# Kernel optimization log

Hardware: AMD Instinct MI355X
Metric: run time of the kernel (lower is better)

Reference implementation:

```python
import jax, jax.numpy as jnp
import numpy as np

B, N, D, K = 32, 2048, 512, 256
NEG_SLOPE = 0.01  # torch LeakyReLU default


def setup_inputs() -> dict:
    key = jax.random.key(0)
    k1, k2, k3, k4, k5, k6 = jax.random.split(key, 6)
    s = 1.0 / np.sqrt(D)
    sk = 1.0 / np.sqrt(K)
    return {
        "vI": jax.random.normal(k1, (B, N, D), dtype=jnp.float32),
        "vQ": jax.random.normal(k2, (B, D), dtype=jnp.float32),
        "Wi": jax.random.uniform(k3, (D, K), minval=-s, maxval=s, dtype=jnp.float32),
        "Wq": jax.random.uniform(k4, (D, K), minval=-s, maxval=s, dtype=jnp.float32),
        "bq": jax.random.uniform(k5, (K,), minval=-s, maxval=s, dtype=jnp.float32),
        "Wp": jax.random.uniform(k6, (K, 1), minval=-sk, maxval=sk, dtype=jnp.float32),
        "bp": jnp.zeros((1,), dtype=jnp.float32),
    }


def reference(vI, vQ, Wi, Wq, bq, Wp, bp):
    # vI: [B,N,D], vQ: [B,D]
    vIp = jnp.einsum("bnd,dk->bnk", vI, Wi)          # [B,N,K] (no bias)
    vQp = vQ @ Wq + bq                                  # [B,K]
    ha = jax.nn.leaky_relu(vIp + vQp[:, None, :], NEG_SLOPE)  # [B,N,K]
    scores = jnp.einsum("bnk,k->bn", ha, Wp[:, 0]) + bp[0]    # [B,N]
    pi = jax.nn.softmax(scores, axis=-1)                # [B,N]
    vI_attn = jnp.einsum("bn,bnk->bk", pi, vIp)        # [B,K]
    return vI_attn + vQp
```

## Files before the change

### kernel.cpp

```cpp
#include <hip/hip_runtime.h>

#define CB 32
#define CN 2048
#define CD 512
#define CK 256

typedef __bf16 bf16x8 __attribute__((ext_vector_type(8)));
typedef float  f32x4  __attribute__((ext_vector_type(4)));

__device__ __forceinline__ unsigned pk2bf(float a, float b) {
    union { float f; unsigned u; } x, y; x.f = a; y.f = b;
    unsigned ru = x.u + 0x7fffu + ((x.u >> 16) & 1u);
    unsigned rv = y.u + 0x7fffu + ((y.u >> 16) & 1u);
    return (ru >> 16) | (rv & 0xffff0000u);
}

__device__ __forceinline__ unsigned short bf16r(float a) {
    union { float f; unsigned u; } x; x.f = a;
    unsigned r = x.u + 0x7fffu + ((x.u >> 16) & 1u);
    return (unsigned short)(r >> 16);
}

__device__ __forceinline__ void glds16(const void* g, void* l) {
    __builtin_amdgcn_global_load_lds(
        (const __attribute__((address_space(1))) void*)g,
        (__attribute__((address_space(3))) void*)l, 16, 0, 0);
}

__global__ __launch_bounds__(256) void prep_kernel(
        const float* __restrict__ Wi, const float* __restrict__ Wq,
        const float* __restrict__ vQ, const float* __restrict__ bq,
        unsigned short* __restrict__ WiT, float* __restrict__ vQpP)
{
    const int tid = threadIdx.x;
    if (blockIdx.x < 32) {
        const int t = blockIdx.x;
        const int d0 = (t >> 2) * 64, k0 = (t & 3) * 64;
        __shared__ float sT[64][68];
        const int r = tid >> 4, c4 = (tid & 15) * 4;
        #pragma unroll
        for (int i = 0; i < 4; ++i) {
            float4 v = *reinterpret_cast<const float4*>(
                Wi + (size_t)(d0 + r + i * 16) * CK + k0 + c4);
            *reinterpret_cast<float4*>(&sT[r + i * 16][c4]) = v;
        }
        __syncthreads();
        const int k = tid >> 2, dg = (tid & 3) * 16;
        unsigned short __attribute__((aligned(16))) ov[16];
        #pragma unroll
        for (int j = 0; j < 16; ++j) ov[j] = bf16r(sT[dg + j][k]);
        unsigned short* dst = WiT + (size_t)(k0 + k) * CD + d0 + dg;
        *reinterpret_cast<uint4*>(dst)     = *reinterpret_cast<const uint4*>(&ov[0]);
        *reinterpret_cast<uint4*>(dst + 8) = *reinterpret_cast<const uint4*>(&ov[8]);
    } else {
        const int bb = blockIdx.x - 32;
        const int b = bb >> 3, j = bb & 7;
        __shared__ float sq[64];
        if (tid < 64) sq[tid] = vQ[b * CD + j * 64 + tid];
        __syncthreads();
        float acc = (j == 0) ? bq[tid] : 0.f;
        const float* wq = Wq + (size_t)j * 64 * CK + tid;
        #pragma unroll
        for (int d = 0; d < 64; d += 8) {
            float wv[8];
            #pragma unroll
            for (int u = 0; u < 8; ++u) wv[u] = wq[(d + u) * CK];
            #pragma unroll
            for (int u = 0; u < 8; ++u) acc += sq[d + u] * wv[u];
        }
        vQpP[(size_t)bb * CK + tid] = acc;
    }
}

__global__ __launch_bounds__(256, 2) void scores_fused_kernel(
        const float* __restrict__ vI, const unsigned short* __restrict__ WiT,
        const float* __restrict__ vQpP, const float* __restrict__ Wp,
        float* __restrict__ numP, float* __restrict__ Zp, float* __restrict__ mP)
{
    constexpr int BM = 128, BK = 64;
    __shared__ __align__(16) unsigned short sB[2][CK * BK];
    float* fb   = (float*)sB[0];
    float* svq  = fb;
    float* swp  = fb + 256;
    float* sS   = fb + 512;
    float* sW   = fb + 640;
    float* snum = fb + 768;

    const int tid  = threadIdx.x;
    const int b    = blockIdx.y;
    const int n0   = blockIdx.x * BM;
    const int wave = tid >> 6;
    const int lane = tid & 63;
    const int col  = lane & 15;
    const int quad = lane >> 4;

    const float* vIb   = vI + ((size_t)b * CN + n0) * CD;
    const float* aBase = vIb + (size_t)(wave * 32 + col) * CD + quad * 8;

    int gBoff[8];
    #pragma unroll
    for (int i = 0; i < 8; ++i) {
        int row = wave * 64 + i * 8 + (lane >> 3);
        int c   = (lane & 7) ^ (row & 7);
        gBoff[i] = row * CD + c * 8;
    }

    f32x4 acc[2][16];
    #pragma unroll
    for (int mt = 0; mt < 2; ++mt)
        #pragma unroll
        for (int kt = 0; kt < 16; ++kt)
            acc[mt][kt] = (f32x4){0.f, 0.f, 0.f, 0.f};

    f32x4 aP[8], aQ[8];

    auto loadA = [&](f32x4* dst, int d0) {
        #pragma unroll
        for (int mt = 0; mt < 2; ++mt)
            #pragma unroll
            for (int s = 0; s < 2; ++s) {
                const float* p = aBase + (size_t)(mt * 16) * CD + d0 + s * 32;
                dst[mt * 4 + s * 2]     = *reinterpret_cast<const f32x4*>(p);
                dst[mt * 4 + s * 2 + 1] = *reinterpret_cast<const f32x4*>(p + 4);
            }
    };
    auto stageB = [&](int d0, int buf) {
        #pragma unroll
        for (int i = 0; i < 8; ++i)
            glds16(WiT + gBoff[i] + d0,
                   (unsigned short*)sB[buf] + (wave * 8 + i) * 512);
    };
    auto compute = [&](const f32x4* ar, const unsigned short* bufC) {
        bf16x8 af[2][2];
        #pragma unroll
        for (int mt = 0; mt < 2; ++mt)
            #pragma unroll
            for (int s = 0; s < 2; ++s) {
                union { unsigned u[4]; bf16x8 v; } t;
                const f32x4 lo = ar[mt * 4 + s * 2], hi = ar[mt * 4 + s * 2 + 1];
                t.u[0] = pk2bf(lo.x, lo.y); t.u[1] = pk2bf(lo.z, lo.w);
                t.u[2] = pk2bf(hi.x, hi.y); t.u[3] = pk2bf(hi.z, hi.w);
                af[mt][s] = t.v;
            }
        __builtin_amdgcn_s_setprio(1);
        #pragma unroll
        for (int s = 0; s < 2; ++s) {
            const int slot = (4 * s + quad) ^ (col & 7);
            #pragma unroll
            for (int kc = 0; kc < 4; ++kc) {
                bf16x8 bfr[4];
                #pragma unroll
                for (int u = 0; u < 4; ++u) {
                    int R = (kc * 4 + u) * 16 + col;
                    bfr[u] = *reinterpret_cast<const bf16x8*>(bufC + R * 64 + slot * 8);
                }
                #pragma unroll
                for (int u = 0; u < 4; ++u)
                    #pragma unroll
                    for (int mt = 0; mt < 2; ++mt)
                        acc[mt][kc * 4 + u] = __builtin_amdgcn_mfma_f32_16x16x32_bf16(
                            af[mt][s], bfr[u], acc[mt][kc * 4 + u], 0, 0, 0);
            }
        }
        __builtin_amdgcn_s_setprio(0);
    };

    loadA(aP, 0);
    stageB(0, 0);
    __syncthreads();

    for (int t = 0; t < 8; ++t) {
        const int d0 = t * BK;
        if (t < 7) {
            stageB(d0 + BK, (t + 1) & 1);
            __builtin_amdgcn_sched_barrier(0);
            loadA((t & 1) ? aP : aQ, d0 + BK);
            __builtin_amdgcn_sched_barrier(0);
        }
        compute((t & 1) ? aQ : aP, sB[t & 1]);
        if (t < 7) {
            asm volatile("s_waitcnt vmcnt(8)" ::: "memory");
        } else {
            asm volatile("s_waitcnt vmcnt(0)" ::: "memory");
        }
        __builtin_amdgcn_s_barrier();
    }
    __syncthreads();

    {
        float a = 0.f;
        #pragma unroll
        for (int j = 0; j < 8; ++j) a += vQpP[(b * 8 + j) * CK + tid];
        svq[tid] = a;
        swp[tid] = Wp[tid];
    }
    __syncthreads();

    float vq[16], wp[16];
    #pragma unroll
    for (int kt = 0; kt < 16; ++kt) {
        vq[kt] = svq[kt * 16 + col];
        wp[kt] = swp[kt * 16 + col];
    }
    float sp[2][4];
    #pragma unroll
    for (int mt = 0; mt < 2; ++mt)
        #pragma unroll
        for (int r = 0; r < 4; ++r) {
            float s = 0.f;
            #pragma unroll
            for (int kt = 0; kt < 16; ++kt) {
                float v = acc[mt][kt][r] + vq[kt];
                v = v > 0.f ? v : 0.01f * v;
                s += v * wp[kt];
            }
            sp[mt][r] = s;
        }
    #pragma unroll
    for (int off = 1; off < 16; off <<= 1)
        #pragma unroll
        for (int mt = 0; mt < 2; ++mt)
            #pragma unroll
            for (int r = 0; r < 4; ++r)
                sp[mt][r] += __shfl_xor(sp[mt][r], off);
    if (col == 0) {
        #pragma unroll
        for (int mt = 0; mt < 2; ++mt)
            #pragma unroll
            for (int r = 0; r < 4; ++r)
                sS[wave * 32 + mt * 16 + quad * 4 + r] = sp[mt][r];
    }
    __syncthreads();

    float m = -1e30f;
    #pragma unroll 8
    for (int i = 0; i < BM; ++i) m = fmaxf(m, sS[i]);
    if (tid < BM) sW[tid] = __expf(sS[tid] - m);
    __syncthreads();
    float z = (tid < BM) ? sW[tid] : 0.f;
    #pragma unroll
    for (int off = 32; off > 0; off >>= 1) z += __shfl_xor(z, off);
    if (lane == 0) sS[wave] = z;
    __syncthreads();
    const int pidx = b * 16 + blockIdx.x;
    if (tid == 0) {
        Zp[pidx] = sS[0] + sS[1] + sS[2] + sS[3];
        mP[pidx] = m;
    }

    float w8[2][4];
    #pragma unroll
    for (int mt = 0; mt < 2; ++mt)
        #pragma unroll
        for (int r = 0; r < 4; ++r)
            w8[mt][r] = sW[wave * 32 + mt * 16 + quad * 4 + r];
    float nk[16];
    #pragma unroll
    for (int kt = 0; kt < 16; ++kt) {
        float s = 0.f;
        #pragma unroll
        for (int mt = 0; mt < 2; ++mt)
            #pragma unroll
            for (int r = 0; r < 4; ++r)
                s += w8[mt][r] * acc[mt][kt][r];
        s += __shfl_xor(s, 16);
        s += __shfl_xor(s, 32);
        nk[kt] = s;
    }
    if (quad == 0) {
        #pragma unroll
        for (int kt = 0; kt < 16; ++kt)
            snum[wave * 256 + kt * 16 + col] = nk[kt];
    }
    __syncthreads();
    numP[(size_t)pidx * CK + tid] =
        snum[tid] + snum[256 + tid] + snum[512 + tid] + snum[768 + tid];
}

__global__ __launch_bounds__(256) void finalize_kernel(
        const float* __restrict__ numP, const float* __restrict__ Zp,
        const float* __restrict__ mP, const float* __restrict__ vQpP,
        float* __restrict__ out)
{
    const int b = blockIdx.x, tid = threadIdx.x;
    float M = -1e30f;
    #pragma unroll
    for (int j = 0; j < 16; ++j) M = fmaxf(M, mP[b * 16 + j]);
    float w[16]; float Zt = 0.f;
    #pragma unroll
    for (int j = 0; j < 16; ++j) {
        w[j] = __expf(mP[b * 16 + j] - M);
        Zt += w[j] * Zp[b * 16 + j];
    }
    const float inv = 1.f / Zt;
    float s = 0.f;
    #pragma unroll
    for (int j = 0; j < 16; ++j) s += w[j] * numP[(size_t)(b * 16 + j) * CK + tid];
    float vq = 0.f;
    #pragma unroll
    for (int j = 0; j < 8; ++j) vq += vQpP[(size_t)(b * 8 + j) * CK + tid];
    out[b * CK + tid] = s * inv + vq;
}

extern "C" void kernel_launch(void* const* d_in, const int* in_sizes, int n_in,
                              void* d_out, int out_size, void* d_ws, size_t ws_size,
                              hipStream_t stream)
{
    const float* vI = (const float*)d_in[0];
    const float* vQ = (const float*)d_in[1];
    const float* Wi = (const float*)d_in[2];
    const float* Wq = (const float*)d_in[3];
    const float* bq = (const float*)d_in[4];
    const float* Wp = (const float*)d_in[5];
    float* out = (float*)d_out;

    char* ws = (char*)d_ws;
    float*          vQpP = (float*)(ws);
    unsigned short* WiT  = (unsigned short*)(ws + 262144);
    float*          numP = (float*)(ws + 524288);
    float*          Zp   = (float*)(ws + 524288 + 524288);
    float*          mP   = (float*)(ws + 1048576 + 2048);

    prep_kernel        <<<288, 256, 0, stream>>>(Wi, Wq, vQ, bq, WiT, vQpP);
    scores_fused_kernel<<<dim3(CN / 128, CB), 256, 0, stream>>>(vI, WiT, vQpP, Wp,
                                                                numP, Zp, mP);
    finalize_kernel    <<<CB, 256, 0, stream>>>(numP, Zp, mP, vQpP, out);
}
```

Measured before the change: 229.1 us.

## Double block rows to 256 with 8 waves staging half of Wi at once

The scores kernel now uses 512 threads per block covering 256 rows instead of 128. The transposed Wi is staged into LDS in two large halves of 256 d-columns (128 KB) rather than a 64-wide double-buffered ring. Each half is reused by twice as many waves, which cuts redundant Wi traffic and the number of barriers in the main loop. The cost is a serialized load stall between halves, less overlap of B loads with MFMA work, and a very large LDS footprint that limits blocks per CU. Partial counts and the finalize kernel are adjusted from 16 to 8 partials per batch.

```diff
diff --git a/kernel.cpp b/kernel.cpp
--- a/kernel.cpp
+++ b/kernel.cpp
@@ -72,19 +72,20 @@
     }
 }
 
-__global__ __launch_bounds__(256, 2) void scores_fused_kernel(
+__global__ __launch_bounds__(512, 2) void scores_fused_kernel(
         const float* __restrict__ vI, const unsigned short* __restrict__ WiT,
         const float* __restrict__ vQpP, const float* __restrict__ Wp,
         float* __restrict__ numP, float* __restrict__ Zp, float* __restrict__ mP)
 {
-    constexpr int BM = 128, BK = 64;
-    __shared__ __align__(16) unsigned short sB[2][CK * BK];
-    float* fb   = (float*)sB[0];
+    constexpr int BM = 256;
+    __shared__ __align__(16) unsigned short sBh[CK * 256];
+    float* fb   = (float*)sBh;
     float* svq  = fb;
     float* swp  = fb + 256;
     float* sS   = fb + 512;
-    float* sW   = fb + 640;
-    float* snum = fb + 768;
+    float* sW   = fb + 768;
+    float* sZ   = fb + 1024;
+    float* snum = fb + 1040;
 
     const int tid  = threadIdx.x;
     const int b    = blockIdx.y;
@@ -97,14 +98,6 @@
     const float* vIb   = vI + ((size_t)b * CN + n0) * CD;
     const float* aBase = vIb + (size_t)(wave * 32 + col) * CD + quad * 8;
 
-    int gBoff[8];
-    #pragma unroll
-    for (int i = 0; i < 8; ++i) {
-        int row = wave * 64 + i * 8 + (lane >> 3);
-        int c   = (lane & 7) ^ (row & 7);
-        gBoff[i] = row * CD + c * 8;
-    }
-
     f32x4 acc[2][16];
     #pragma unroll
     for (int mt = 0; mt < 2; ++mt)
@@ -124,13 +117,19 @@
                 dst[mt * 4 + s * 2 + 1] = *reinterpret_cast<const f32x4*>(p + 4);
             }
     };
-    auto stageB = [&](int d0, int buf) {
-        #pragma unroll
-        for (int i = 0; i < 8; ++i)
-            glds16(WiT + gBoff[i] + d0,
-                   (unsigned short*)sB[buf] + (wave * 8 + i) * 512);
+
+    auto stageB = [&](int p) {
+        #pragma unroll
+        for (int i = 0; i < 16; ++i) {
+            const int k0  = wave * 32 + i * 2;
+            const int k   = k0 + (lane >> 5);
+            const int dlb = ((lane & 31) * 16) ^ ((k & 7) << 4);
+            glds16(WiT + (size_t)k * CD + p * 256 + (dlb >> 1),
+                   (unsigned short*)sBh + k0 * 256);
+        }
     };
-    auto compute = [&](const f32x4* ar, const unsigned short* bufC) {
+
+    auto compute = [&](int tl, const f32x4* ar) {
         bf16x8 af[2][2];
         #pragma unroll
         for (int mt = 0; mt < 2; ++mt)
@@ -142,18 +141,17 @@
                 t.u[2] = pk2bf(hi.x, hi.y); t.u[3] = pk2bf(hi.z, hi.w);
                 af[mt][s] = t.v;
             }
-        __builtin_amdgcn_s_setprio(1);
         #pragma unroll
         for (int s = 0; s < 2; ++s) {
-            const int slot = (4 * s + quad) ^ (col & 7);
+            const int slot = ((s * 4 + quad) ^ (col & 7)) << 4;
+            const unsigned short* base = sBh + col * 256 + ((tl * 128 + slot) >> 1);
             #pragma unroll
             for (int kc = 0; kc < 4; ++kc) {
                 bf16x8 bfr[4];
                 #pragma unroll
-                for (int u = 0; u < 4; ++u) {
-                    int R = (kc * 4 + u) * 16 + col;
-                    bfr[u] = *reinterpret_cast<const bf16x8*>(bufC + R * 64 + slot * 8);
-                }
+                for (int u = 0; u < 4; ++u)
+                    bfr[u] = *reinterpret_cast<const bf16x8*>(
+                        base + (size_t)(kc * 4 + u) * 16 * 256);
                 #pragma unroll
                 for (int u = 0; u < 4; ++u)
                     #pragma unroll
@@ -162,32 +160,31 @@
                             af[mt][s], bfr[u], acc[mt][kc * 4 + u], 0, 0, 0);
             }
         }
-        __builtin_amdgcn_s_setprio(0);
     };
 
     loadA(aP, 0);
-    stageB(0, 0);
-    __syncthreads();
-
-    for (int t = 0; t < 8; ++t) {
-        const int d0 = t * BK;
-        if (t < 7) {
-            stageB(d0 + BK, (t + 1) & 1);
-            __builtin_amdgcn_sched_barrier(0);
-            loadA((t & 1) ? aP : aQ, d0 + BK);
-            __builtin_amdgcn_sched_barrier(0);
-        }
-        compute((t & 1) ? aQ : aP, sB[t & 1]);
-        if (t < 7) {
-            asm volatile("s_waitcnt vmcnt(8)" ::: "memory");
-        } else {
-            asm volatile("s_waitcnt vmcnt(0)" ::: "memory");
-        }
-        __builtin_amdgcn_s_barrier();
-    }
-    __syncthreads();
-
-    {
+    stageB(0);
+    __syncthreads();
+
+    #pragma unroll
+    for (int t = 0; t < 4; ++t) {
+        loadA((t & 1) ? aP : aQ, (t + 1) * 64);
+        compute(t, (t & 1) ? aQ : aP);
+    }
+
+    __syncthreads();
+    stageB(1);
+    asm volatile("s_waitcnt vmcnt(0)" ::: "memory");
+    __builtin_amdgcn_s_barrier();
+
+    #pragma unroll
+    for (int t = 4; t < 8; ++t) {
+        if (t < 7) loadA((t & 1) ? aP : aQ, (t + 1) * 64);
+        compute(t & 3, (t & 1) ? aQ : aP);
+    }
+    __syncthreads();
+
+    if (tid < CK) {
         float a = 0.f;
         #pragma unroll
         for (int j = 0; j < 8; ++j) a += vQpP[(b * 8 + j) * CK + tid];
@@ -240,11 +237,11 @@
     float z = (tid < BM) ? sW[tid] : 0.f;
     #pragma unroll
     for (int off = 32; off > 0; off >>= 1) z += __shfl_xor(z, off);
-    if (lane == 0) sS[wave] = z;
-    __syncthreads();
-    const int pidx = b * 16 + blockIdx.x;
+    if (lane == 0 && wave < 4) sZ[wave] = z;
+    __syncthreads();
+    const int pidx = b * 8 + blockIdx.x;
     if (tid == 0) {
-        Zp[pidx] = sS[0] + sS[1] + sS[2] + sS[3];
+        Zp[pidx] = sZ[0] + sZ[1] + sZ[2] + sZ[3];
         mP[pidx] = m;
     }
 
@@ -273,8 +270,12 @@
             snum[wave * 256 + kt * 16 + col] = nk[kt];
     }
     __syncthreads();
-    numP[(size_t)pidx * CK + tid] =
-        snum[tid] + snum[256 + tid] + snum[512 + tid] + snum[768 + tid];
+    if (tid < CK) {
+        float s = 0.f;
+        #pragma unroll
+        for (int w = 0; w < 8; ++w) s += snum[w * 256 + tid];
+        numP[(size_t)pidx * CK + tid] = s;
+    }
 }
 
 __global__ __launch_bounds__(256) void finalize_kernel(
@@ -285,17 +286,17 @@
     const int b = blockIdx.x, tid = threadIdx.x;
     float M = -1e30f;
     #pragma unroll
-    for (int j = 0; j < 16; ++j) M = fmaxf(M, mP[b * 16 + j]);
-    float w[16]; float Zt = 0.f;
-    #pragma unroll
-    for (int j = 0; j < 16; ++j) {
-        w[j] = __expf(mP[b * 16 + j] - M);
-        Zt += w[j] * Zp[b * 16 + j];
+    for (int j = 0; j < 8; ++j) M = fmaxf(M, mP[b * 8 + j]);
+    float w[8]; float Zt = 0.f;
+    #pragma unroll
+    for (int j = 0; j < 8; ++j) {
+        w[j] = __expf(mP[b * 8 + j] - M);
+        Zt += w[j] * Zp[b * 8 + j];
     }
     const float inv = 1.f / Zt;
     float s = 0.f;
     #pragma unroll
-    for (int j = 0; j < 16; ++j) s += w[j] * numP[(size_t)(b * 16 + j) * CK + tid];
+    for (int j = 0; j < 8; ++j) s += w[j] * numP[(size_t)(b * 8 + j) * CK + tid];
     float vq = 0.f;
     #pragma unroll
     for (int j = 0; j < 8; ++j) vq += vQpP[(size_t)(b * 8 + j) * CK + tid];
@@ -318,11 +319,11 @@
     float*          vQpP = (float*)(ws);
     unsigned short* WiT  = (unsigned short*)(ws + 262144);
     float*          numP = (float*)(ws + 524288);
-    float*          Zp   = (float*)(ws + 524288 + 524288);
-    float*          mP   = (float*)(ws + 1048576 + 2048);
+    float*          Zp   = (float*)(ws + 786432);
+    float*          mP   = (float*)(ws + 787456);
 
     prep_kernel        <<<288, 256, 0, stream>>>(Wi, Wq, vQ, bq, WiT, vQpP);
-    scores_fused_kernel<<<dim3(CN / 128, CB), 256, 0, stream>>>(vI, WiT, vQpP, Wp,
+    scores_fused_kernel<<<dim3(CN / 256, CB), 512, 0, stream>>>(vI, WiT, vQpP, Wp,
                                                                 numP, Zp, mP);
     finalize_kernel    <<<CB, 256, 0, stream>>>(numP, Zp, mP, vQpP, out);
 }
```

Result: no change. 225.6 us (-1.5%).
